# Optimization experiments

Measured on AMD Instinct MI355X. Metric: run time of the kernel, lower is better.

The kernel has to match this reference:

```python
import jax, jax.numpy as jnp
import numpy as np

ANCHORS = jnp.array([1.3221, 1.73145, 3.19275, 4.00944, 5.05587,
                     8.09892, 9.47112, 4.84053, 11.2364, 10.0071], dtype=jnp.float32)
GRID, NA, NC, CH = 13, 5, 20, 25  # grid size, anchors, classes, channels per anchor


def setup_inputs() -> dict:
    key = jax.random.key(0)
    k1, k2, k3 = jax.random.split(key, 3)
    B, O = 2048, 32
    det = jax.random.normal(k1, (B, NA * CH, GRID, GRID), dtype=jnp.float32)
    gt_boxes = jax.random.uniform(k2, (B, O, 4), dtype=jnp.float32)  # x,y,w,h in [0,1)
    gt_class = jax.random.randint(k3, (B, O), 0, NC)
    return {"detection_result": det, "gt_boxes": gt_boxes, "gt_class": gt_class}


def _forward(det, gt_boxes, gt_class):
    B, O = gt_boxes.shape[0], gt_boxes.shape[1]
    d = det.reshape(B, NA, CH, GRID, GRID)
    # scale predicted w,h by anchor priors / grid (the in-place loop in torch)
    wh = ANCHORS.reshape(NA, 2) / GRID
    scale = jnp.ones((NA, CH), det.dtype).at[:, 2:4].set(wh)
    d = d * scale[None, :, :, None, None]

    N = B * O
    gb = gt_boxes.reshape(N, 4)
    x, y, w, h = gb[:, 0], gb[:, 1], gb[:, 2], gb[:, 3]
    cls = gt_class.reshape(N)
    b_idx = jnp.repeat(jnp.arange(B), O)
    gx = jnp.floor(x * GRID).astype(jnp.int32)
    gy = jnp.floor(y * GRID).astype(jnp.int32)

    # gather the 5 anchor-box predictions at each object's cell: [N, 5, 4]
    pred = d[b_idx, :, :4, gy, gx]
    px, py, pw, ph = pred[..., 0], pred[..., 1], pred[..., 2], pred[..., 3]
    bx0 = (px + gx[:, None]) / GRID - pw / 2
    by0 = (py + gy[:, None]) / GRID - ph / 2
    bx1, by1 = bx0 + pw, by0 + ph
    gx0, gy0 = (x - w / 2)[:, None], (y - h / 2)[:, None]
    gx1, gy1 = (x + w / 2)[:, None], (y + h / 2)[:, None]
    ix0 = jnp.maximum(gx0, bx0); iy0 = jnp.maximum(gy0, by0)
    ix1 = jnp.minimum(gx1, bx1); iy1 = jnp.minimum(gy1, by1)
    inter = (ix1 - ix0 + 1) * (iy1 - iy0 + 1)  # faithful +1 from source
    a1 = (gx1 - gx0 + 1) * (gy1 - gy0 + 1)
    a2 = (bx1 - bx0 + 1) * (by1 - by0 + 1)
    iou = inter / (a1 + a2 - inter)
    aidx = jnp.argmax(iou, axis=1).astype(jnp.int32)  # best anchor per object

    tx, ty = x * GRID - gx, y * GRID - gy
    onehot = jax.nn.one_hot(cls, NC, dtype=det.dtype)
    vals = jnp.concatenate(
        [jnp.stack([tx, ty, w, h, jnp.ones_like(x)], axis=1), onehot], axis=1)  # [N,25]
    wvals = jnp.concatenate(
        [jnp.array([5., 5., 5., 5., 1.]), jnp.ones(NC)]).astype(det.dtype)

    # sequential torch writes deterministically
    S = B * NA * GRID * GRID
    flat = ((b_idx * NA + aidx) * GRID + gy) * GRID + gx
    owner = jnp.full((S,), -1, jnp.int32).at[flat].max(jnp.arange(N, dtype=jnp.int32))
    valid = owner >= 0
    gt_slot = jnp.where(valid[:, None], vals[jnp.clip(owner, 0)], 0.0)  # [S,25]
    w_slot = jnp.where(valid[:, None], wvals[None, :], 0.0)
    gt_grid = gt_slot.reshape(B, NA, GRID, GRID, CH).transpose(0, 1, 4, 2, 3)
    weight = w_slot.reshape(B, NA, GRID, GRID, CH).transpose(0, 1, 4, 2, 3)

    obj = gt_grid[:, :, 4] == 1.0  # [B,5,13,13]
    weight = weight.at[:, :, 4].set(jnp.where(obj, weight[:, :, 4], 0.5))

    wse = weight * (gt_grid - d) ** 2
    loss = jnp.sum(wse)
    obj_f = obj.astype(det.dtype)
    obj_loss = jnp.sum(obj_f[:, :, None] * wse[:, :, 0:5])
    no_obj_loss = jnp.sum((1.0 - obj_f) * wse[:, :, 4])
    conf_loss = jnp.sum(obj_f[:, :, None] * wse[:, :, 5:25])
    return loss, obj_loss, no_obj_loss, conf_loss


def reference(detection_result, gt_boxes, gt_class):
    return _forward(detection_result, gt_boxes, gt_class)
```

## Files before the change

### kernel.cpp

```cpp
#include <hip/hip_runtime.h>

#define GRIDSZ 13
#define NANCH  5
#define NCHAN  25
#define BATCH  2048
#define NOBJ   32
#define PLANE  (GRIDSZ * GRIDSZ)
#define NTOT   (BATCH * NOBJ)
#define NCHUNK (BATCH * NANCH)
#define ABLOCKS 256
#define BBLOCKS 256
#define TBLOCKS (ABLOCKS + BBLOCKS)

__constant__ float AW[NANCH] = {1.3221f / 13.0f, 3.19275f / 13.0f, 5.05587f / 13.0f,
                                9.47112f / 13.0f, 11.2364f / 13.0f};
__constant__ float AH[NANCH] = {1.73145f / 13.0f, 4.00944f / 13.0f, 8.09892f / 13.0f,
                                4.84053f / 13.0f, 10.0071f / 13.0f};

__global__ void main_kernel(const float* __restrict__ det,
                            const float* __restrict__ gt_boxes,
                            const int* __restrict__ gt_class,
                            float4* __restrict__ partials) {
    __shared__ int flats[256];
    __shared__ float sm[4][4];
    float loss = 0.0f, objl = 0.0f, noobjl = 0.0f, confl = 0.0f;

    if (blockIdx.x < ABLOCKS) {
        int n = blockIdx.x * 256 + threadIdx.x;
        int b = n >> 5;
        float4 g = ((const float4*)gt_boxes)[n];
        float x = g.x, y = g.y, w = g.z, h = g.w;
        int gx = (int)floorf(x * 13.0f);
        int gy = (int)floorf(y * 13.0f);

        float gx0 = x - w * 0.5f, gy0 = y - h * 0.5f;
        float gx1 = x + w * 0.5f, gy1 = y + h * 0.5f;
        float a1 = (gx1 - gx0 + 1.0f) * (gy1 - gy0 + 1.0f);

        const float* cell = det + (size_t)b * (NANCH * NCHAN) * PLANE + gy * GRIDSZ + gx;

        float best = -INFINITY;
        int aidx = 0;
        float c0 = 0.f, c1 = 0.f, c2 = 0.f, c3 = 0.f;
        #pragma unroll
        for (int a = 0; a < NANCH; ++a) {
            const float* p = cell + (size_t)a * NCHAN * PLANE;
            float px = p[0];
            float py = p[PLANE];
            float pw = p[2 * PLANE] * AW[a];
            float ph = p[3 * PLANE] * AH[a];
            float bx0 = (px + (float)gx) / 13.0f - pw * 0.5f;
            float by0 = (py + (float)gy) / 13.0f - ph * 0.5f;
            float bx1 = bx0 + pw, by1 = by0 + ph;
            float ix0 = fmaxf(gx0, bx0), iy0 = fmaxf(gy0, by0);
            float ix1 = fminf(gx1, bx1), iy1 = fminf(gy1, by1);
            float inter = (ix1 - ix0 + 1.0f) * (iy1 - iy0 + 1.0f);
            float a2 = (bx1 - bx0 + 1.0f) * (by1 - by0 + 1.0f);
            float iou = inter / (a1 + a2 - inter);
            if (iou > best) { best = iou; aidx = a; c0 = px; c1 = py; c2 = pw; c3 = ph; }
        }
        int flat = ((b * NANCH + aidx) * GRIDSZ + gy) * GRIDSZ + gx;

        flats[threadIdx.x] = flat;
        __syncthreads();
        int o  = threadIdx.x & 31;
        int bb = threadIdx.x & ~31;
        bool winner = true;
        for (int m = o + 1; m < 32; ++m)
            if (flats[bb + m] == flat) winner = false;

        if (winner) {
            const float* p = cell + (size_t)aidx * NCHAN * PLANE;
            float d4 = p[4 * PLANE];
            int cls = gt_class[n];
            float tx = x * 13.0f - (float)gx;
            float ty = y * 13.0f - (float)gy;
            float e, t, corr = 0.0f;
            e = tx - c0;   t = 5.0f * e * e; corr += t; objl += t;
            e = ty - c1;   t = 5.0f * e * e; corr += t; objl += t;
            e = w  - c2;   t = 5.0f * e * e; corr += t; objl += t;
            e = h  - c3;   t = 5.0f * e * e; corr += t; objl += t;
            e = 1.0f - d4; t = e * e;        corr += t; objl += t;
            #pragma unroll
            for (int c = 5; c < NCHAN; ++c) {
                float gtv = (c - 5 == cls) ? 1.0f : 0.0f;
                e = gtv - p[c * PLANE];
                t = e * e;
                corr += t;
                confl += t;
            }
            float sub = 0.5f * d4 * d4;
            loss   = corr - sub;
            noobjl = -sub;
        }
    } else {
        int wid = threadIdx.x >> 6, lane = threadIdx.x & 63;
        int wglob = (blockIdx.x - ABLOCKS) * 4 + wid;
        float s = 0.0f;
        for (int chunk = wglob; chunk < NCHUNK; chunk += BBLOCKS * 4) {
            const float* p = det + (size_t)chunk * (NCHAN * PLANE) + 4 * PLANE;
            for (int i = lane; i < PLANE; i += 64) {
                float d = p[i];
                s += d * d;
            }
        }
        loss   = 0.5f * s;
        noobjl = 0.5f * s;
    }

    #pragma unroll
    for (int off = 32; off > 0; off >>= 1) {
        loss   += __shfl_down(loss, off);
        objl   += __shfl_down(objl, off);
        noobjl += __shfl_down(noobjl, off);
        confl  += __shfl_down(confl, off);
    }
    int lane = threadIdx.x & 63;
    int wid  = threadIdx.x >> 6;
    __syncthreads();
    if (lane == 0) {
        sm[wid][0] = loss; sm[wid][1] = objl; sm[wid][2] = noobjl; sm[wid][3] = confl;
    }
    __syncthreads();
    if (threadIdx.x == 0) {
        float s0 = 0, s1 = 0, s2 = 0, s3 = 0;
        #pragma unroll
        for (int i = 0; i < 4; ++i) {
            s0 += sm[i][0]; s1 += sm[i][1]; s2 += sm[i][2]; s3 += sm[i][3];
        }
        partials[blockIdx.x] = make_float4(s0, s1, s2, s3);
    }
}

__global__ void reduce_kernel(const float4* __restrict__ partials,
                              float* __restrict__ out) {
    float s0 = 0, s1 = 0, s2 = 0, s3 = 0;
    for (int i = threadIdx.x; i < TBLOCKS; i += 256) {
        float4 v = partials[i];
        s0 += v.x; s1 += v.y; s2 += v.z; s3 += v.w;
    }
    #pragma unroll
    for (int off = 32; off > 0; off >>= 1) {
        s0 += __shfl_down(s0, off);
        s1 += __shfl_down(s1, off);
        s2 += __shfl_down(s2, off);
        s3 += __shfl_down(s3, off);
    }
    __shared__ float sm[4][4];
    int lane = threadIdx.x & 63;
    int wid  = threadIdx.x >> 6;
    if (lane == 0) {
        sm[wid][0] = s0; sm[wid][1] = s1; sm[wid][2] = s2; sm[wid][3] = s3;
    }
    __syncthreads();
    if (threadIdx.x == 0) {
        float a0 = 0, a1 = 0, a2 = 0, a3 = 0;
        #pragma unroll
        for (int i = 0; i < 4; ++i) {
            a0 += sm[i][0]; a1 += sm[i][1]; a2 += sm[i][2]; a3 += sm[i][3];
        }
        out[0] = a0; out[1] = a1; out[2] = a2; out[3] = a3;
    }
}

extern "C" void kernel_launch(void* const* d_in, const int* in_sizes, int n_in,
                              void* d_out, int out_size, void* d_ws, size_t ws_size,
                              hipStream_t stream) {
    const float* det = (const float*)d_in[0];
    const float* gtb = (const float*)d_in[1];
    const int*   gtc = (const int*)d_in[2];
    float* out = (float*)d_out;
    float4* partials = (float4*)d_ws;

    main_kernel<<<TBLOCKS, 256, 0, stream>>>(det, gtb, gtc, partials);
    reduce_kernel<<<1, 256, 0, stream>>>(partials, out);
}
```

Measured before the change: 32.51 us.

## Restructure to one block per batch image with per-anchor and per-class threads

Replaces the split design, where some blocks handled objects and others summed confidence planes, with one 256-thread block per batch image. Each block computes IoU with one thread per object-anchor pair, reduces argmax and winners through shared memory, and spreads the 20 class-channel gathers across threads. It also sums that image's confidence planes in the same block. This exposes more memory-level parallelism for the scattered gathers, at the cost of more blocks, several barriers, and many idle threads in the per-object phases.

```diff
diff --git a/kernel.cpp b/kernel.cpp
--- a/kernel.cpp
+++ b/kernel.cpp
@@ -6,106 +6,129 @@
 #define BATCH  2048
 #define NOBJ   32
 #define PLANE  (GRIDSZ * GRIDSZ)
-#define NTOT   (BATCH * NOBJ)
-#define NCHUNK (BATCH * NANCH)
-#define ABLOCKS 256
-#define BBLOCKS 256
-#define TBLOCKS (ABLOCKS + BBLOCKS)
 
 __constant__ float AW[NANCH] = {1.3221f / 13.0f, 3.19275f / 13.0f, 5.05587f / 13.0f,
                                 9.47112f / 13.0f, 11.2364f / 13.0f};
 __constant__ float AH[NANCH] = {1.73145f / 13.0f, 4.00944f / 13.0f, 8.09892f / 13.0f,
                                 4.84053f / 13.0f, 10.0071f / 13.0f};
 
-__global__ void main_kernel(const float* __restrict__ det,
-                            const float* __restrict__ gt_boxes,
-                            const int* __restrict__ gt_class,
-                            float4* __restrict__ partials) {
-    __shared__ int flats[256];
-    __shared__ float sm[4][4];
+__global__ void __launch_bounds__(256) main_kernel(const float* __restrict__ det,
+                                                   const float* __restrict__ gt_boxes,
+                                                   const int* __restrict__ gt_class,
+                                                   float4* __restrict__ partials) {
+    int b = blockIdx.x;
+    int t = threadIdx.x;
+    __shared__ float  iou_sm[NOBJ * NANCH];
+    __shared__ float4 pred_sm[NOBJ * NANCH];
+    __shared__ float4 box_sm[NOBJ];
+    __shared__ int    gx_sm[NOBJ], gy_sm[NOBJ];
+    __shared__ int    cls_sm[NOBJ];
+    __shared__ int    flat_sm[NOBJ];
+    __shared__ int    aidx_sm[NOBJ];
+    __shared__ int    win_sm[NOBJ];
+    __shared__ float  sm4[4][4];
+
+    const float* detb = det + (size_t)b * (NANCH * NCHAN) * PLANE;
+
     float loss = 0.0f, objl = 0.0f, noobjl = 0.0f, confl = 0.0f;
 
-    if (blockIdx.x < ABLOCKS) {
-        int n = blockIdx.x * 256 + threadIdx.x;
-        int b = n >> 5;
-        float4 g = ((const float4*)gt_boxes)[n];
+    if (t < NOBJ * NANCH) {
+        int gt = t / NANCH, a = t - gt * NANCH;
+        float4 g = ((const float4*)gt_boxes)[b * NOBJ + gt];
         float x = g.x, y = g.y, w = g.z, h = g.w;
         int gx = (int)floorf(x * 13.0f);
         int gy = (int)floorf(y * 13.0f);
-
+        if (a == 0) {
+            gx_sm[gt] = gx; gy_sm[gt] = gy;
+            box_sm[gt] = g;
+            cls_sm[gt] = gt_class[b * NOBJ + gt];
+        }
+        const float* p = detb + (size_t)a * NCHAN * PLANE + gy * GRIDSZ + gx;
+        float px = p[0];
+        float py = p[PLANE];
+        float pw = p[2 * PLANE] * AW[a];
+        float ph = p[3 * PLANE] * AH[a];
         float gx0 = x - w * 0.5f, gy0 = y - h * 0.5f;
         float gx1 = x + w * 0.5f, gy1 = y + h * 0.5f;
         float a1 = (gx1 - gx0 + 1.0f) * (gy1 - gy0 + 1.0f);
+        float bx0 = (px + (float)gx) / 13.0f - pw * 0.5f;
+        float by0 = (py + (float)gy) / 13.0f - ph * 0.5f;
+        float bx1 = bx0 + pw, by1 = by0 + ph;
+        float ix0 = fmaxf(gx0, bx0), iy0 = fmaxf(gy0, by0);
+        float ix1 = fminf(gx1, bx1), iy1 = fminf(gy1, by1);
+        float inter = (ix1 - ix0 + 1.0f) * (iy1 - iy0 + 1.0f);
+        float a2 = (bx1 - bx0 + 1.0f) * (by1 - by0 + 1.0f);
+        iou_sm[t] = inter / (a1 + a2 - inter);
+        pred_sm[t] = make_float4(px, py, pw, ph);
+    }
 
-        const float* cell = det + (size_t)b * (NANCH * NCHAN) * PLANE + gy * GRIDSZ + gx;
+    {
+        float s = 0.0f;
+        for (int idx = t; idx < NANCH * PLANE; idx += 256) {
+            int a = idx / PLANE, i = idx - a * PLANE;
+            float d = detb[((size_t)a * NCHAN + 4) * PLANE + i];
+            s += d * d;
+        }
+        loss += 0.5f * s;
+        noobjl += 0.5f * s;
+    }
 
+    __syncthreads();
+
+    if (t < NOBJ) {
         float best = -INFINITY;
         int aidx = 0;
-        float c0 = 0.f, c1 = 0.f, c2 = 0.f, c3 = 0.f;
         #pragma unroll
         for (int a = 0; a < NANCH; ++a) {
-            const float* p = cell + (size_t)a * NCHAN * PLANE;
-            float px = p[0];
-            float py = p[PLANE];
-            float pw = p[2 * PLANE] * AW[a];
-            float ph = p[3 * PLANE] * AH[a];
-            float bx0 = (px + (float)gx) / 13.0f - pw * 0.5f;
-            float by0 = (py + (float)gy) / 13.0f - ph * 0.5f;
-            float bx1 = bx0 + pw, by1 = by0 + ph;
-            float ix0 = fmaxf(gx0, bx0), iy0 = fmaxf(gy0, by0);
-            float ix1 = fminf(gx1, bx1), iy1 = fminf(gy1, by1);
-            float inter = (ix1 - ix0 + 1.0f) * (iy1 - iy0 + 1.0f);
-            float a2 = (bx1 - bx0 + 1.0f) * (by1 - by0 + 1.0f);
-            float iou = inter / (a1 + a2 - inter);
-            if (iou > best) { best = iou; aidx = a; c0 = px; c1 = py; c2 = pw; c3 = ph; }
+            float v = iou_sm[t * NANCH + a];
+            if (v > best) { best = v; aidx = a; }
         }
-        int flat = ((b * NANCH + aidx) * GRIDSZ + gy) * GRIDSZ + gx;
+        aidx_sm[t] = aidx;
+        flat_sm[t] = (aidx * GRIDSZ + gy_sm[t]) * GRIDSZ + gx_sm[t];
+    }
+    __syncthreads();
 
-        flats[threadIdx.x] = flat;
-        __syncthreads();
-        int o  = threadIdx.x & 31;
-        int bb = threadIdx.x & ~31;
-        bool winner = true;
-        for (int m = o + 1; m < 32; ++m)
-            if (flats[bb + m] == flat) winner = false;
+    if (t < NOBJ) {
+        int f = flat_sm[t];
+        int winner = 1;
+        for (int m = t + 1; m < NOBJ; ++m)
+            if (flat_sm[m] == f) winner = 0;
+        win_sm[t] = winner;
+    }
+    __syncthreads();
 
-        if (winner) {
-            const float* p = cell + (size_t)aidx * NCHAN * PLANE;
-            float d4 = p[4 * PLANE];
-            int cls = gt_class[n];
-            float tx = x * 13.0f - (float)gx;
-            float ty = y * 13.0f - (float)gy;
-            float e, t, corr = 0.0f;
-            e = tx - c0;   t = 5.0f * e * e; corr += t; objl += t;
-            e = ty - c1;   t = 5.0f * e * e; corr += t; objl += t;
-            e = w  - c2;   t = 5.0f * e * e; corr += t; objl += t;
-            e = h  - c3;   t = 5.0f * e * e; corr += t; objl += t;
-            e = 1.0f - d4; t = e * e;        corr += t; objl += t;
-            #pragma unroll
-            for (int c = 5; c < NCHAN; ++c) {
-                float gtv = (c - 5 == cls) ? 1.0f : 0.0f;
-                e = gtv - p[c * PLANE];
-                t = e * e;
-                corr += t;
-                confl += t;
-            }
-            float sub = 0.5f * d4 * d4;
-            loss   = corr - sub;
-            noobjl = -sub;
+    if (t < NOBJ && win_sm[t]) {
+        int aidx = aidx_sm[t];
+        float4 pr = pred_sm[t * NANCH + aidx];
+        float4 g = box_sm[t];
+        int gx = gx_sm[t], gy = gy_sm[t];
+        const float* p = detb + (size_t)aidx * NCHAN * PLANE + gy * GRIDSZ + gx;
+        float d4 = p[4 * PLANE];
+        float tx = g.x * 13.0f - (float)gx;
+        float ty = g.y * 13.0f - (float)gy;
+        float e, tt, corr = 0.0f;
+        e = tx - pr.x;  tt = 5.0f * e * e; corr += tt; objl += tt;
+        e = ty - pr.y;  tt = 5.0f * e * e; corr += tt; objl += tt;
+        e = g.z - pr.z; tt = 5.0f * e * e; corr += tt; objl += tt;
+        e = g.w - pr.w; tt = 5.0f * e * e; corr += tt; objl += tt;
+        e = 1.0f - d4;  tt = e * e;        corr += tt; objl += tt;
+        float sub = 0.5f * d4 * d4;
+        loss += corr - sub;
+        noobjl -= sub;
+    }
+
+    for (int item = t; item < NOBJ * 20; item += 256) {
+        int gt = item / 20;
+        int c = 5 + (item - gt * 20);
+        if (win_sm[gt]) {
+            int aidx = aidx_sm[gt];
+            float d = detb[((size_t)aidx * NCHAN + c) * PLANE + gy_sm[gt] * GRIDSZ + gx_sm[gt]];
+            float gtv = (c - 5 == cls_sm[gt]) ? 1.0f : 0.0f;
+            float e = gtv - d;
+            float tt = e * e;
+            loss += tt;
+            confl += tt;
         }
-    } else {
-        int wid = threadIdx.x >> 6, lane = threadIdx.x & 63;
-        int wglob = (blockIdx.x - ABLOCKS) * 4 + wid;
-        float s = 0.0f;
-        for (int chunk = wglob; chunk < NCHUNK; chunk += BBLOCKS * 4) {
-            const float* p = det + (size_t)chunk * (NCHAN * PLANE) + 4 * PLANE;
-            for (int i = lane; i < PLANE; i += 64) {
-                float d = p[i];
-                s += d * d;
-            }
-        }
-        loss   = 0.5f * s;
-        noobjl = 0.5f * s;
     }
 
     #pragma unroll
@@ -115,18 +138,17 @@
         noobjl += __shfl_down(noobjl, off);
         confl  += __shfl_down(confl, off);
     }
-    int lane = threadIdx.x & 63;
-    int wid  = threadIdx.x >> 6;
-    __syncthreads();
+    int lane = t & 63;
+    int wid  = t >> 6;
     if (lane == 0) {
-        sm[wid][0] = loss; sm[wid][1] = objl; sm[wid][2] = noobjl; sm[wid][3] = confl;
+        sm4[wid][0] = loss; sm4[wid][1] = objl; sm4[wid][2] = noobjl; sm4[wid][3] = confl;
     }
     __syncthreads();
-    if (threadIdx.x == 0) {
+    if (t == 0) {
         float s0 = 0, s1 = 0, s2 = 0, s3 = 0;
         #pragma unroll
         for (int i = 0; i < 4; ++i) {
-            s0 += sm[i][0]; s1 += sm[i][1]; s2 += sm[i][2]; s3 += sm[i][3];
+            s0 += sm4[i][0]; s1 += sm4[i][1]; s2 += sm4[i][2]; s3 += sm4[i][3];
         }
         partials[blockIdx.x] = make_float4(s0, s1, s2, s3);
     }
@@ -135,7 +157,7 @@
 __global__ void reduce_kernel(const float4* __restrict__ partials,
                               float* __restrict__ out) {
     float s0 = 0, s1 = 0, s2 = 0, s3 = 0;
-    for (int i = threadIdx.x; i < TBLOCKS; i += 256) {
+    for (int i = threadIdx.x; i < BATCH; i += 256) {
         float4 v = partials[i];
         s0 += v.x; s1 += v.y; s2 += v.z; s3 += v.w;
     }
@@ -172,6 +194,6 @@
     float* out = (float*)d_out;
     float4* partials = (float4*)d_ws;
 
-    main_kernel<<<TBLOCKS, 256, 0, stream>>>(det, gtb, gtc, partials);
+    main_kernel<<<BATCH, 256, 0, stream>>>(det, gtb, gtc, partials);
     reduce_kernel<<<1, 256, 0, stream>>>(partials, out);
 }
```

New measurement: 33.43 us. 1.03x slower.
